# Kernel tuning notes

Hardware: AMD Instinct MI355X
Metric: run time of the kernel (lower is better)

The kernel has to match this reference:

```python
import jax, jax.numpy as jnp
import numpy as np

T, B, E, H = 1024, 8, 1024, 16
DH = E // H
MASKED_BIAS = -10000.0


def setup_inputs() -> dict:
    key = jax.random.key(0)
    k1, k2, k3 = jax.random.split(key, 3)
    query = jax.random.normal(k1, (T, B, E), dtype=jnp.float32)
    # xavier-uniform-ish scale for the fused QKV and output projections
    qkv_w = jax.random.normal(k2, (3 * E, E), dtype=jnp.float32) * (1.0 / np.sqrt(2.0 * E))
    out_w = jax.random.normal(k3, (E, E), dtype=jnp.float32) * (1.0 / np.sqrt(E))
    return {
        "query": query,
        "qkv_w": qkv_w,
        "qkv_b": jnp.zeros((3 * E,), jnp.float32),
        "out_w": out_w,
        "out_b": jnp.zeros((E,), jnp.float32),
    }


def reference(query, qkv_w, qkv_b, out_w, out_b):
    # query: [T, B, E] (Time x Batch x Channel, fairseq convention)
    tgt_len, bsz, embed_dim = query.shape
    scaling = DH ** (-0.5)

    # Fused QKV projection (QuantLinear fake-quant treated as identity numerics)
    qkv = jnp.einsum("tbe,fe->tbf", query, qkv_w) + qkv_b  # [T, B, 3E]
    q, k, v = jnp.split(qkv, 3, axis=-1)
    q = q * scaling

    def to_heads(x):  # [T, B, E] -> [B*H, T, DH]
        return x.reshape(tgt_len, bsz * H, DH).transpose(1, 0, 2)

    q, k, v = to_heads(q), to_heads(k), to_heads(v)

    # attn_weights: [B*H, T, S]
    attn_weights = jnp.einsum("ntd,nsd->nts", q, k)

    # causal mask from the tril `bias` buffer with masked_bias fill
    causal = jnp.tril(jnp.ones((tgt_len, tgt_len), dtype=bool))
    attn_weights = jnp.where(causal[None, :, :], attn_weights,
                             jnp.asarray(MASKED_BIAS, attn_weights.dtype))

    attn_probs = jax.nn.softmax(attn_weights, axis=-1)
    # dropout p=0.0 in eval: no-op

    attn = jnp.einsum("nts,nsd->ntd", attn_probs, v)  # [B*H, T, DH]
    attn = attn.transpose(1, 0, 2).reshape(tgt_len, bsz, embed_dim)  # [T, B, E]

    out = jnp.einsum("tbe,fe->tbf", attn, out_w) + out_b
    return out
```

## Files before the change

### kernel.cpp

```cpp
#include <hip/hip_runtime.h>

typedef __attribute__((ext_vector_type(4))) float f32x4;
typedef __attribute__((ext_vector_type(16))) float f32x16;
typedef __attribute__((ext_vector_type(8))) short bf16x8;
typedef __attribute__((ext_vector_type(4))) unsigned short u16x4;
typedef __attribute__((ext_vector_type(4))) unsigned int u32x4;

#define T_DIM 1024
#define B_DIM 8
#define E_DIM 1024
#define H_DIM 16
#define DH 64

__device__ __forceinline__ unsigned short f2bf(float f) {
  unsigned int u = __builtin_bit_cast(unsigned int, f);
  u += 0x7fffu + ((u >> 16) & 1u);
  return (unsigned short)(u >> 16);
}

__device__ __forceinline__ unsigned int cvtpk_bf16(float lo, float hi) {
  unsigned int r;
  asm("v_cvt_pk_bf16_f32 %0, %1, %2" : "=v"(r) : "v"(lo), "v"(hi));
  return r;
}

__device__ __forceinline__ float exp2_hw(float x) {
  float r;
  asm("v_exp_f32 %0, %1" : "=v"(r) : "v"(x));
  return r;
}

__device__ __forceinline__ f32x4 mfma16(bf16x8 a, bf16x8 b, f32x4 c) {
  return __builtin_amdgcn_mfma_f32_16x16x32_bf16(a, b, c, 0, 0, 0);
}
__device__ __forceinline__ f32x16 mfma32(bf16x8 a, bf16x8 b, f32x16 c) {
  return __builtin_amdgcn_mfma_f32_32x32x16_bf16(a, b, c, 0, 0, 0);
}

__global__ __launch_bounds__(256) void cast_f32_to_bf16(
    const float* __restrict__ src, unsigned short* __restrict__ dst, int n4) {
  int i = blockIdx.x * 256 + threadIdx.x;
  if (i >= n4) return;
  f32x4 v = *(const f32x4*)(src + (size_t)i * 4);
  u16x4 o;
  o[0] = f2bf(v[0]); o[1] = f2bf(v[1]); o[2] = f2bf(v[2]); o[3] = f2bf(v[3]);
  *(u16x4*)(dst + (size_t)i * 4) = o;
}

__device__ __forceinline__ void mainloop_128x128(
    const unsigned short* __restrict__ Ab,
    const unsigned short* __restrict__ Bb,
    unsigned short* smem, f32x4 acc[4][4]) {
  const int tid = threadIdx.x;
  const int wave = tid >> 6, lane = tid & 63;
  const int lr = lane & 15, lg = lane >> 4;
  const int x7 = lr & 7;
  const int wr = wave >> 1, wc = wave & 1;
  const int rlo = lane >> 3;
  const int csw = 8 * ((lane & 7) ^ rlo);

#define STG(KT, BUF)                                                            \
  {                                                                             \
    unsigned short* la_ = smem + (BUF) * 16384;                                 \
    unsigned short* lb_ = la_ + 8192;                                           \
    _Pragma("unroll")                                                           \
    for (int c_ = 0; c_ < 4; ++c_) {                                            \
      const int ins_ = wave * 4 + c_;                                           \
      __builtin_amdgcn_global_load_lds(                                         \
          (const __attribute__((address_space(1))) void*)(Ab + (size_t)(ins_ * 8 + rlo) * 1024 + (KT) * 64 + csw), \
          (__attribute__((address_space(3))) void*)(la_ + ins_ * 512), 16, 0, 0); \
      __builtin_amdgcn_global_load_lds(                                         \
          (const __attribute__((address_space(1))) void*)(Bb + (size_t)(ins_ * 8 + rlo) * 1024 + (KT) * 64 + csw), \
          (__attribute__((address_space(3))) void*)(lb_ + ins_ * 512), 16, 0, 0); \
    }                                                                           \
  }

#define COMPUTE(BUF)                                                            \
  {                                                                             \
    const unsigned short* la_ = smem + (BUF) * 16384;                           \
    const unsigned short* ha_ = la_ + (wr * 64) * 64;                           \
    const unsigned short* hb_ = la_ + 8192 + (wc * 64) * 64;                    \
    _Pragma("unroll")                                                           \
    for (int ks_ = 0; ks_ < 2; ++ks_) {                                         \
      bf16x8 af_[4], bf_[4];                                                    \
      const int cu_ = (((ks_ * 4 + lg) ^ x7) << 3);                             \
      _Pragma("unroll")                                                         \
      for (int i_ = 0; i_ < 4; ++i_) {                                          \
        af_[i_] = *(const bf16x8*)(ha_ + (i_ * 16 + lr) * 64 + cu_);            \
        bf_[i_] = *(const bf16x8*)(hb_ + (i_ * 16 + lr) * 64 + cu_);            \
      }                                                                         \
      __builtin_amdgcn_s_setprio(1);                                            \
      _Pragma("unroll")                                                         \
      for (int mi_ = 0; mi_ < 4; ++mi_)                                         \
        _Pragma("unroll")                                                       \
        for (int ni_ = 0; ni_ < 4; ++ni_)                                       \
          acc[mi_][ni_] = mfma16(af_[mi_], bf_[ni_], acc[mi_][ni_]);            \
      __builtin_amdgcn_s_setprio(0);                                            \
    }                                                                           \
  }

  STG(0, 0)
  __syncthreads();
#pragma unroll 4
  for (int t = 0; t < 16; ++t) {
    if (t < 15) STG(t + 1, (t + 1) & 1)
    COMPUTE(t & 1)
    __syncthreads();
  }
#undef STG
#undef COMPUTE
}

__global__ __launch_bounds__(256) void gemm_qkv10(
    const unsigned short* __restrict__ A, const unsigned short* __restrict__ W,
    const float* __restrict__ bias,
    unsigned short* __restrict__ Qh, unsigned short* __restrict__ Kh,
    unsigned short* __restrict__ Vh) {
  __shared__ unsigned short smem[32768];
  const int bid = blockIdx.x;
  const int swz = (bid & 7) * 192 + (bid >> 3);
  const int m0 = (swz & 63) * 128;
  const int n0 = (swz >> 6) * 128;

  f32x4 acc[4][4];
  const f32x4 z4 = {0.f, 0.f, 0.f, 0.f};
#pragma unroll
  for (int i = 0; i < 4; ++i)
#pragma unroll
    for (int j = 0; j < 4; ++j) acc[i][j] = z4;

  mainloop_128x128(A + (size_t)m0 * 1024, W + (size_t)n0 * 1024, smem, acc);

  const int lane = threadIdx.x & 63, wave = threadIdx.x >> 6;
  const int lr = lane & 15, lg = lane >> 4;
  const int wr = wave >> 1, wc = wave & 1;
#pragma unroll
  for (int mf = 0; mf < 4; ++mf)
#pragma unroll
    for (int nf = 0; nf < 4; ++nf)
#pragma unroll
      for (int j = 0; j < 4; ++j) {
        int m = m0 + wr * 64 + mf * 16 + lg * 4 + j;
        int f = n0 + wc * 64 + nf * 16 + lr;
        float v = acc[mf][nf][j] + bias[f];
        int t = m >> 3, b = m & 7;
        int e = f & 1023, h = e >> 6, d = e & 63;
        int which = f >> 10;
        size_t idx = ((size_t)(b * 16 + h) * T_DIM + t) * DH + d;
        if (which == 0)      Qh[idx] = f2bf(v * 0.18033688011111772f);
        else if (which == 1) Kh[idx] = f2bf(v);
        else                 Vh[idx] = f2bf(v);
      }
}

__global__ __launch_bounds__(256) void gemm_out10(
    const unsigned short* __restrict__ A, const unsigned short* __restrict__ W,
    const float* __restrict__ bias, float* __restrict__ out) {
  __shared__ unsigned short smem[32768];
  const int bid = blockIdx.x;
  const int swz = (bid & 7) * 64 + (bid >> 3);
  const int m0 = (swz & 63) * 128;
  const int n0 = (swz >> 6) * 128;

  f32x4 acc[4][4];
  const f32x4 z4 = {0.f, 0.f, 0.f, 0.f};
#pragma unroll
  for (int i = 0; i < 4; ++i)
#pragma unroll
    for (int j = 0; j < 4; ++j) acc[i][j] = z4;

  mainloop_128x128(A + (size_t)m0 * 1024, W + (size_t)n0 * 1024, smem, acc);

  const int lane = threadIdx.x & 63, wave = threadIdx.x >> 6;
  const int lr = lane & 15, lg = lane >> 4;
  const int wr = wave >> 1, wc = wave & 1;
#pragma unroll
  for (int mf = 0; mf < 4; ++mf)
#pragma unroll
    for (int nf = 0; nf < 4; ++nf)
#pragma unroll
      for (int j = 0; j < 4; ++j) {
        int m = m0 + wr * 64 + mf * 16 + lg * 4 + j;
        int f = n0 + wc * 64 + nf * 16 + lr;
        out[(size_t)m * E_DIM + f] = acc[mf][nf][j] + bias[f];
      }
}

__global__ __launch_bounds__(256) void transpose_v(
    const unsigned short* __restrict__ Vh, unsigned short* __restrict__ Vt) {
  __shared__ unsigned short tile[64][72];
  const int n = blockIdx.x, t0 = blockIdx.y * 64;
  const int tid = threadIdx.x;
  const int r = tid >> 3, c8 = tid & 7;
#pragma unroll
  for (int it = 0; it < 2; ++it) {
    int row = it * 32 + r;
    bf16x8 v = *(const bf16x8*)(Vh + ((size_t)n * T_DIM + t0 + row) * DH + c8 * 8);
    *(bf16x8*)&tile[row][c8 * 8] = v;
  }
  __syncthreads();
#pragma unroll
  for (int it = 0; it < 2; ++it) {
    int d = it * 32 + r;
    bf16x8 ov;
#pragma unroll
    for (int jj = 0; jj < 8; ++jj) ov[jj] = (short)tile[c8 * 8 + jj][d];
    *(bf16x8*)(Vt + ((size_t)n * DH + d) * T_DIM + t0 + c8 * 8) = ov;
  }
}

__global__ __launch_bounds__(256) void flash_attn6(
    const unsigned short* __restrict__ Qh, const unsigned short* __restrict__ Kh,
    const unsigned short* __restrict__ Vt, unsigned short* __restrict__ attn) {
  __shared__ unsigned short lds[2][2][4096];
  const int tid = threadIdx.x;
  const int wave = tid >> 6, lane = tid & 63;
  const int lq = lane & 31, hi = lane >> 5;
  const int bid = blockIdx.x;
  const int qt = 7 - (bid >> 7);
  const int n = bid & 127;
  const int b = n >> 4, h = n & 15;
  const int q0w = qt * 128 + wave * 32;
  const int q = q0w + lq;
  const int nbb = 2 * qt + 2;
  const int mynb = (q0w + 95) >> 6;

  const unsigned short* kh_n = Kh + (size_t)n * (T_DIM * DH);
  const unsigned short* vt_n = Vt + (size_t)n * (DH * T_DIM);

  const int rlo = lane >> 3;
  const int csw = 8 * ((lane & 7) ^ rlo);

#define STAGE(S0, BUF)                                                          \
  {                                                                             \
    _Pragma("unroll")                                                           \
    for (int m_ = 0; m_ < 2; ++m_) {                                            \
      const int instr_ = wave * 2 + m_;                                         \
      const int r_ = instr_ * 8 + rlo;                                          \
      __builtin_amdgcn_global_load_lds(                                         \
          (const __attribute__((address_space(1))) void*)(kh_n + (size_t)((S0) + r_) * DH + csw), \
          (__attribute__((address_space(3))) void*)(&lds[BUF][0][instr_ * 512]), 16, 0, 0); \
      __builtin_amdgcn_global_load_lds(                                         \
          (const __attribute__((address_space(1))) void*)(vt_n + (size_t)r_ * T_DIM + (S0) + csw), \
          (__attribute__((address_space(3))) void*)(&lds[BUF][1][instr_ * 512]), 16, 0, 0); \
    }                                                                           \
  }

  bf16x8 qf[4];
  const unsigned short* qp = Qh + ((size_t)n * T_DIM + q) * DH + hi * 8;
#pragma unroll
  for (int kk = 0; kk < 4; ++kk) qf[kk] = *(const bf16x8*)(qp + kk * 16);

  f32x16 o0, o1;
#pragma unroll
  for (int r = 0; r < 16; ++r) { o0[r] = 0.f; o1[r] = 0.f; }
  float m_run = -1e30f, l_run = 0.f;

  STAGE(0, 0);
  asm volatile("s_waitcnt vmcnt(0)");
  __builtin_amdgcn_s_barrier();

  const int swzr = (lq & 7) << 4;

  for (int i = 0; i < nbb; ++i) {
    const int cur = i & 1;
    if (i + 1 < nbb) {
      STAGE((i + 1) * 64, cur ^ 1);
      asm volatile("s_waitcnt vmcnt(4)");
    } else {
      asm volatile("s_waitcnt vmcnt(0)");
    }
    __builtin_amdgcn_s_barrier();
    __builtin_amdgcn_sched_barrier(0);

    if (i < mynb) {
      const int s0 = i * 64;
      const unsigned short* kb = lds[cur][0];
      const unsigned short* vb = lds[cur][1];
      f32x16 sA, sB;
#pragma unroll
      for (int r = 0; r < 16; ++r) { sA[r] = 0.f; sB[r] = 0.f; }
      __builtin_amdgcn_s_setprio(1);
#pragma unroll
      for (int kk = 0; kk < 4; ++kk) {
        const int cb = ((kk * 32 + hi * 16) ^ swzr) >> 1;
        bf16x8 ka = *(const bf16x8*)(kb + lq * 64 + cb);
        bf16x8 kbf = *(const bf16x8*)(kb + (32 + lq) * 64 + cb);
        sA = mfma32(ka, qf[kk], sA);
        sB = mfma32(kbf, qf[kk], sB);
      }
      __builtin_amdgcn_s_setprio(0);
      if (i == mynb - 1) {
#pragma unroll
        for (int r = 0; r < 16; ++r) {
          int sp = s0 + (r & 3) + 8 * (r >> 2) + 4 * hi;
          if (sp > q)      sA[r] = -10000.0f;
          if (sp + 32 > q) sB[r] = -10000.0f;
        }
      }
      float t0 = fmaxf(sA[0], sB[0]), t1 = fmaxf(sA[1], sB[1]);
      float t2 = fmaxf(sA[2], sB[2]), t3 = fmaxf(sA[3], sB[3]);
#pragma unroll
      for (int r = 4; r < 16; r += 4) {
        t0 = fmaxf(t0, fmaxf(sA[r], sB[r]));
        t1 = fmaxf(t1, fmaxf(sA[r + 1], sB[r + 1]));
        t2 = fmaxf(t2, fmaxf(sA[r + 2], sB[r + 2]));
        t3 = fmaxf(t3, fmaxf(sA[r + 3], sB[r + 3]));
      }
      float tmax = fmaxf(fmaxf(t0, t1), fmaxf(t2, t3));
      tmax = fmaxf(tmax, __shfl_xor(tmax, 32));
      if (__any(tmax - m_run > 11.5f)) {
        float m_new = fmaxf(m_run, tmax);
        float sc = exp2_hw(m_run - m_new);
        l_run *= sc;
#pragma unroll
        for (int r = 0; r < 16; ++r) { o0[r] *= sc; o1[r] *= sc; }
        m_run = m_new;
      }
      float r0 = 0.f, r1 = 0.f, r2 = 0.f, r3 = 0.f;
#pragma unroll
      for (int r = 0; r < 16; r += 4) {
        sA[r] = exp2_hw(sA[r] - m_run);         r0 += sA[r];
        sA[r + 1] = exp2_hw(sA[r + 1] - m_run); r1 += sA[r + 1];
        sA[r + 2] = exp2_hw(sA[r + 2] - m_run); r2 += sA[r + 2];
        sA[r + 3] = exp2_hw(sA[r + 3] - m_run); r3 += sA[r + 3];
      }
#pragma unroll
      for (int r = 0; r < 16; r += 4) {
        sB[r] = exp2_hw(sB[r] - m_run);         r0 += sB[r];
        sB[r + 1] = exp2_hw(sB[r + 1] - m_run); r1 += sB[r + 1];
        sB[r + 2] = exp2_hw(sB[r + 2] - m_run); r2 += sB[r + 2];
        sB[r + 3] = exp2_hw(sB[r + 3] - m_run); r3 += sB[r + 3];
      }
      float rs = (r0 + r1) + (r2 + r3);
      rs += __shfl_xor(rs, 32);
      l_run += rs;
      unsigned int pk[16];
#pragma unroll
      for (int ii = 0; ii < 8; ++ii) pk[ii]     = cvtpk_bf16(sA[2 * ii], sA[2 * ii + 1]);
#pragma unroll
      for (int ii = 0; ii < 8; ++ii) pk[8 + ii] = cvtpk_bf16(sB[2 * ii], sB[2 * ii + 1]);
      __builtin_amdgcn_s_setprio(1);
#pragma unroll
      for (int ks = 0; ks < 4; ++ks) {
        unsigned int A0 = pk[ks * 4 + 0], A1 = pk[ks * 4 + 1];
        unsigned int B0 = pk[ks * 4 + 2], B1 = pk[ks * 4 + 3];
        unsigned int xA0 = __shfl_xor(A0, 32), xA1 = __shfl_xor(A1, 32);
        unsigned int xB0 = __shfl_xor(B0, 32), xB1 = __shfl_xor(B1, 32);
        u32x4 uu;
        uu[0] = hi ? xB0 : A0;
        uu[1] = hi ? xB1 : A1;
        uu[2] = hi ? B0 : xA0;
        uu[3] = hi ? B1 : xA1;
        bf16x8 pf = __builtin_bit_cast(bf16x8, uu);
        const int cb = ((ks * 32 + hi * 16) ^ swzr) >> 1;
        bf16x8 v0 = *(const bf16x8*)(vb + lq * 64 + cb);
        bf16x8 v1 = *(const bf16x8*)(vb + (32 + lq) * 64 + cb);
        o0 = mfma32(v0, pf, o0);
        o1 = mfma32(v1, pf, o1);
      }
      __builtin_amdgcn_s_setprio(0);
    }
    __builtin_amdgcn_s_barrier();
  }
#undef STAGE

  const float inv = 1.0f / l_run;
  unsigned short* op = attn + ((size_t)q * B_DIM + b) * E_DIM + h * DH;
#pragma unroll
  for (int g = 0; g < 4; ++g) {
    u16x4 w0, w1;
#pragma unroll
    for (int jj = 0; jj < 4; ++jj) {
      w0[jj] = f2bf(o0[g * 4 + jj] * inv);
      w1[jj] = f2bf(o1[g * 4 + jj] * inv);
    }
    int d = 8 * g + 4 * hi;
    *(u16x4*)(op + d) = w0;
    *(u16x4*)(op + 32 + d) = w1;
  }
}

extern "C" void kernel_launch(void* const* d_in, const int* in_sizes, int n_in,
                              void* d_out, int out_size, void* d_ws, size_t ws_size,
                              hipStream_t stream) {
  const float* query = (const float*)d_in[0];
  const float* qkv_w = (const float*)d_in[1];
  const float* qkv_b = (const float*)d_in[2];
  const float* out_w = (const float*)d_in[3];
  const float* out_b = (const float*)d_in[4];
  float* out = (float*)d_out;

  char* ws = (char*)d_ws;
  unsigned short* Abf  = (unsigned short*)(ws);
  unsigned short* Wbf  = (unsigned short*)(ws + (size_t)(16u << 20));
  unsigned short* OWbf = (unsigned short*)(ws + (size_t)(22u << 20));
  unsigned short* Qh   = (unsigned short*)(ws + (size_t)(24u << 20));
  unsigned short* Kh   = (unsigned short*)(ws + (size_t)(40u << 20));
  unsigned short* Vh   = (unsigned short*)(ws + (size_t)(56u << 20));
  unsigned short* Vt   = (unsigned short*)(ws + (size_t)(72u << 20));
  unsigned short* attn = Abf;

  cast_f32_to_bf16<<<8192, 256, 0, stream>>>(query, Abf, 8388608 / 4);
  cast_f32_to_bf16<<<3072, 256, 0, stream>>>(qkv_w, Wbf, 3145728 / 4);
  cast_f32_to_bf16<<<1024, 256, 0, stream>>>(out_w, OWbf, 1048576 / 4);
  gemm_qkv10<<<1536, 256, 0, stream>>>(Abf, Wbf, qkv_b, Qh, Kh, Vh);
  transpose_v<<<dim3(128, 16), 256, 0, stream>>>(Vh, Vt);
  flash_attn6<<<1024, 256, 0, stream>>>(Qh, Kh, Vt, attn);
  gemm_out10<<<512, 256, 0, stream>>>(attn, OWbf, out_b, out);
}
```

Baseline: 169.9 us.

## Use 256x128 GEMM tiles with triple-buffered LDS and merge cast kernels

```diff
diff --git a/kernel.cpp b/kernel.cpp
--- a/kernel.cpp
+++ b/kernel.cpp
@@ -37,17 +37,24 @@
   return __builtin_amdgcn_mfma_f32_32x32x16_bf16(a, b, c, 0, 0, 0);
 }
 
-__global__ __launch_bounds__(256) void cast_f32_to_bf16(
-    const float* __restrict__ src, unsigned short* __restrict__ dst, int n4) {
+__global__ __launch_bounds__(256) void cast_all(
+    const float* __restrict__ q, const float* __restrict__ w1,
+    const float* __restrict__ w2, unsigned short* __restrict__ dq,
+    unsigned short* __restrict__ dw1, unsigned short* __restrict__ dw2) {
   int i = blockIdx.x * 256 + threadIdx.x;
-  if (i >= n4) return;
-  f32x4 v = *(const f32x4*)(src + (size_t)i * 4);
+  const float* src;
+  unsigned short* dst;
+  int off;
+  if (i < 2097152)      { src = q;  dst = dq;  off = i; }
+  else if (i < 2883584) { src = w1; dst = dw1; off = i - 2097152; }
+  else                  { src = w2; dst = dw2; off = i - 2883584; }
+  f32x4 v = *(const f32x4*)(src + (size_t)off * 4);
   u16x4 o;
   o[0] = f2bf(v[0]); o[1] = f2bf(v[1]); o[2] = f2bf(v[2]); o[3] = f2bf(v[3]);
-  *(u16x4*)(dst + (size_t)i * 4) = o;
-}
-
-__device__ __forceinline__ void mainloop_128x128(
+  *(u16x4*)(dst + (size_t)off * 4) = o;
+}
+
+__device__ __forceinline__ void mainloop_256x128(
     const unsigned short* __restrict__ Ab,
     const unsigned short* __restrict__ Bb,
     unsigned short* smem, f32x4 acc[4][4]) {
@@ -59,77 +66,137 @@
   const int rlo = lane >> 3;
   const int csw = 8 * ((lane & 7) ^ rlo);
 
-#define STG(KT, BUF)                                                            \
+#define STG_U(KT, WB, U)                                                        \
   {                                                                             \
-    unsigned short* la_ = smem + (BUF) * 16384;                                 \
-    unsigned short* lb_ = la_ + 8192;                                           \
+    const unsigned short* g_ = ((U) == 2) ? Bb : (Ab + (size_t)(U) * 131072);   \
+    unsigned short* l_ = smem + (WB) * 24576 + (((U) == 2) ? 16384 : (U) * 8192); \
     _Pragma("unroll")                                                           \
-    for (int c_ = 0; c_ < 4; ++c_) {                                            \
-      const int ins_ = wave * 4 + c_;                                           \
+    for (int c_ = 0; c_ < 2; ++c_) {                                            \
+      const int ins_ = wave * 2 + c_;                                           \
       __builtin_amdgcn_global_load_lds(                                         \
-          (const __attribute__((address_space(1))) void*)(Ab + (size_t)(ins_ * 8 + rlo) * 1024 + (KT) * 64 + csw), \
-          (__attribute__((address_space(3))) void*)(la_ + ins_ * 512), 16, 0, 0); \
-      __builtin_amdgcn_global_load_lds(                                         \
-          (const __attribute__((address_space(1))) void*)(Bb + (size_t)(ins_ * 8 + rlo) * 1024 + (KT) * 64 + csw), \
-          (__attribute__((address_space(3))) void*)(lb_ + ins_ * 512), 16, 0, 0); \
+          (const __attribute__((address_space(1))) void*)(g_ + (size_t)(ins_ * 8 + rlo) * 1024 + (KT) * 64 + csw), \
+          (__attribute__((address_space(3))) void*)(l_ + ins_ * 512), 16, 0, 0); \
     }                                                                           \
   }
 
-#define COMPUTE(BUF)                                                            \
-  {                                                                             \
-    const unsigned short* la_ = smem + (BUF) * 16384;                           \
-    const unsigned short* ha_ = la_ + (wr * 64) * 64;                           \
-    const unsigned short* hb_ = la_ + 8192 + (wc * 64) * 64;                    \
-    _Pragma("unroll")                                                           \
-    for (int ks_ = 0; ks_ < 2; ++ks_) {                                         \
-      bf16x8 af_[4], bf_[4];                                                    \
-      const int cu_ = (((ks_ * 4 + lg) ^ x7) << 3);                             \
-      _Pragma("unroll")                                                         \
-      for (int i_ = 0; i_ < 4; ++i_) {                                          \
-        af_[i_] = *(const bf16x8*)(ha_ + (i_ * 16 + lr) * 64 + cu_);            \
-        bf_[i_] = *(const bf16x8*)(hb_ + (i_ * 16 + lr) * 64 + cu_);            \
-      }                                                                         \
-      __builtin_amdgcn_s_setprio(1);                                            \
-      _Pragma("unroll")                                                         \
-      for (int mi_ = 0; mi_ < 4; ++mi_)                                         \
-        _Pragma("unroll")                                                       \
-        for (int ni_ = 0; ni_ < 4; ++ni_)                                       \
-          acc[mi_][ni_] = mfma16(af_[mi_], bf_[ni_], acc[mi_][ni_]);            \
-      __builtin_amdgcn_s_setprio(0);                                            \
-    }                                                                           \
-  }
-
-  STG(0, 0)
-  __syncthreads();
-#pragma unroll 4
+#define BAR_IN()                                                                \
+  __builtin_amdgcn_s_barrier();                                                 \
+  asm volatile("s_waitcnt lgkmcnt(0)" ::: "memory");                            \
+  __builtin_amdgcn_sched_barrier(0);
+
+#define BAR_OUT()                                                               \
+  __builtin_amdgcn_s_barrier();                                                 \
+  __builtin_amdgcn_sched_barrier(0);
+
+  STG_U(0, 0, 0) STG_U(0, 0, 1) STG_U(0, 0, 2)
+  STG_U(1, 1, 0) STG_U(1, 1, 1) STG_U(1, 1, 2)
+  asm volatile("s_waitcnt vmcnt(6)" ::: "memory");
+  BAR_OUT()
+
   for (int t = 0; t < 16; ++t) {
-    if (t < 15) STG(t + 1, (t + 1) & 1)
-    COMPUTE(t & 1)
-    __syncthreads();
-  }
-#undef STG
-#undef COMPUTE
-}
-
-__global__ __launch_bounds__(256) void gemm_qkv10(
+    const unsigned short* bA = smem + (t % 3) * 24576;
+    const unsigned short* bB = bA + 16384;
+    const int wb = (t + 2) % 3;
+    const int kt2 = t + 2;
+    const unsigned short* hA = bA + (wr * 64) * 64;
+    const unsigned short* hB = bB + (wc * 64) * 64;
+    bf16x8 af[2], bfr[4];
+
+    {
+      const int cu = (lg ^ x7) << 3;
+      af[0] = *(const bf16x8*)(hA + lr * 64 + cu);
+      af[1] = *(const bf16x8*)(hA + (16 + lr) * 64 + cu);
+#pragma unroll
+      for (int nf = 0; nf < 4; ++nf)
+        bfr[nf] = *(const bf16x8*)(hB + (nf * 16 + lr) * 64 + cu);
+      if (t < 14) STG_U(kt2, wb, 0)
+      BAR_IN()
+      __builtin_amdgcn_s_setprio(1);
+#pragma unroll
+      for (int nf = 0; nf < 4; ++nf) {
+        acc[0][nf] = mfma16(af[0], bfr[nf], acc[0][nf]);
+        acc[1][nf] = mfma16(af[1], bfr[nf], acc[1][nf]);
+      }
+      __builtin_amdgcn_s_setprio(0);
+      BAR_OUT()
+    }
+    {
+      const int cu = (lg ^ x7) << 3;
+      af[0] = *(const bf16x8*)(hA + (32 + lr) * 64 + cu);
+      af[1] = *(const bf16x8*)(hA + (48 + lr) * 64 + cu);
+      if (t < 14) STG_U(kt2, wb, 1)
+      BAR_IN()
+      __builtin_amdgcn_s_setprio(1);
+#pragma unroll
+      for (int nf = 0; nf < 4; ++nf) {
+        acc[2][nf] = mfma16(af[0], bfr[nf], acc[2][nf]);
+        acc[3][nf] = mfma16(af[1], bfr[nf], acc[3][nf]);
+      }
+      __builtin_amdgcn_s_setprio(0);
+      BAR_OUT()
+    }
+    {
+      const int cu = ((4 + lg) ^ x7) << 3;
+      af[0] = *(const bf16x8*)(hA + lr * 64 + cu);
+      af[1] = *(const bf16x8*)(hA + (16 + lr) * 64 + cu);
+#pragma unroll
+      for (int nf = 0; nf < 4; ++nf)
+        bfr[nf] = *(const bf16x8*)(hB + (nf * 16 + lr) * 64 + cu);
+      if (t < 14) STG_U(kt2, wb, 2)
+      BAR_IN()
+      __builtin_amdgcn_s_setprio(1);
+#pragma unroll
+      for (int nf = 0; nf < 4; ++nf) {
+        acc[0][nf] = mfma16(af[0], bfr[nf], acc[0][nf]);
+        acc[1][nf] = mfma16(af[1], bfr[nf], acc[1][nf]);
+      }
+      __builtin_amdgcn_s_setprio(0);
+      BAR_OUT()
+    }
+    {
+      const int cu = ((4 + lg) ^ x7) << 3;
+      af[0] = *(const bf16x8*)(hA + (32 + lr) * 64 + cu);
+      af[1] = *(const bf16x8*)(hA + (48 + lr) * 64 + cu);
+      BAR_IN()
+      __builtin_amdgcn_s_setprio(1);
+#pragma unroll
+      for (int nf = 0; nf < 4; ++nf) {
+        acc[2][nf] = mfma16(af[0], bfr[nf], acc[2][nf]);
+        acc[3][nf] = mfma16(af[1], bfr[nf], acc[3][nf]);
+      }
+      __builtin_amdgcn_s_setprio(0);
+      if (t < 14) {
+        asm volatile("s_waitcnt vmcnt(6)" ::: "memory");
+      } else if (t == 14) {
+        asm volatile("s_waitcnt vmcnt(0)" ::: "memory");
+      }
+      BAR_OUT()
+    }
+  }
+#undef STG_U
+#undef BAR_IN
+#undef BAR_OUT
+}
+
+__global__ __launch_bounds__(512) void gemm_qkv11(
     const unsigned short* __restrict__ A, const unsigned short* __restrict__ W,
     const float* __restrict__ bias,
     unsigned short* __restrict__ Qh, unsigned short* __restrict__ Kh,
     unsigned short* __restrict__ Vh) {
-  __shared__ unsigned short smem[32768];
+  extern __shared__ unsigned short smem[];
   const int bid = blockIdx.x;
-  const int swz = (bid & 7) * 192 + (bid >> 3);
-  const int m0 = (swz & 63) * 128;
-  const int n0 = (swz >> 6) * 128;
+  const int xcd = bid & 7, i = bid >> 3;
+  const int m0 = (xcd * 4 + (i & 3)) * 256;
+  const int n0 = (i >> 2) * 128;
 
   f32x4 acc[4][4];
   const f32x4 z4 = {0.f, 0.f, 0.f, 0.f};
 #pragma unroll
-  for (int i = 0; i < 4; ++i)
-#pragma unroll
-    for (int j = 0; j < 4; ++j) acc[i][j] = z4;
-
-  mainloop_128x128(A + (size_t)m0 * 1024, W + (size_t)n0 * 1024, smem, acc);
+  for (int a = 0; a < 4; ++a)
+#pragma unroll
+    for (int b2 = 0; b2 < 4; ++b2) acc[a][b2] = z4;
+
+  mainloop_256x128(A + (size_t)m0 * 1024, W + (size_t)n0 * 1024, smem, acc);
 
   const int lane = threadIdx.x & 63, wave = threadIdx.x >> 6;
   const int lr = lane & 15, lg = lane >> 4;
@@ -153,23 +220,23 @@
       }
 }
 
-__global__ __launch_bounds__(256) void gemm_out10(
+__global__ __launch_bounds__(512) void gemm_out11(
     const unsigned short* __restrict__ A, const unsigned short* __restrict__ W,
     const float* __restrict__ bias, float* __restrict__ out) {
-  __shared__ unsigned short smem[32768];
+  extern __shared__ unsigned short smem[];
   const int bid = blockIdx.x;
-  const int swz = (bid & 7) * 64 + (bid >> 3);
-  const int m0 = (swz & 63) * 128;
-  const int n0 = (swz >> 6) * 128;
+  const int xcd = bid & 7, i = bid >> 3;
+  const int m0 = (xcd * 4 + (i & 3)) * 256;
+  const int n0 = (i >> 2) * 128;
 
   f32x4 acc[4][4];
   const f32x4 z4 = {0.f, 0.f, 0.f, 0.f};
 #pragma unroll
-  for (int i = 0; i < 4; ++i)
-#pragma unroll
-    for (int j = 0; j < 4; ++j) acc[i][j] = z4;
-
-  mainloop_128x128(A + (size_t)m0 * 1024, W + (size_t)n0 * 1024, smem, acc);
+  for (int a = 0; a < 4; ++a)
+#pragma unroll
+    for (int b2 = 0; b2 < 4; ++b2) acc[a][b2] = z4;
+
+  mainloop_256x128(A + (size_t)m0 * 1024, W + (size_t)n0 * 1024, smem, acc);
 
   const int lane = threadIdx.x & 63, wave = threadIdx.x >> 6;
   const int lr = lane & 15, lg = lane >> 4;
@@ -401,11 +468,9 @@
   unsigned short* Vt   = (unsigned short*)(ws + (size_t)(72u << 20));
   unsigned short* attn = Abf;
 
-  cast_f32_to_bf16<<<8192, 256, 0, stream>>>(query, Abf, 8388608 / 4);
-  cast_f32_to_bf16<<<3072, 256, 0, stream>>>(qkv_w, Wbf, 3145728 / 4);
-  cast_f32_to_bf16<<<1024, 256, 0, stream>>>(out_w, OWbf, 1048576 / 4);
-  gemm_qkv10<<<1536, 256, 0, stream>>>(Abf, Wbf, qkv_b, Qh, Kh, Vh);
+  cast_all<<<12288, 256, 0, stream>>>(query, qkv_w, out_w, Abf, Wbf, OWbf);
+  gemm_qkv11<<<768, 512, 147456, stream>>>(Abf, Wbf, qkv_b, Qh, Kh, Vh);
   transpose_v<<<dim3(128, 16), 256, 0, stream>>>(Vh, Vt);
   flash_attn6<<<1024, 256, 0, stream>>>(Qh, Kh, Vt, attn);
-  gemm_out10<<<512, 256, 0, stream>>>(attn, OWbf, out_b, out);
-}
+  gemm_out11<<<256, 512, 147456, stream>>>(attn, OWbf, out_b, out);
+}
```

Result: faster. 158.9 us (-6.4%).
